# Kernel tuning notes

Measured on AMD Instinct MI355X. Metric: run time of the kernel, lower is better.

Reference implementation:

```python
import jax, jax.numpy as jnp
import numpy as np

N, D, K = 65536, 4096, 16
LN_EPS = 1e-5
SN_EPS = 1e-12
MIN_NORM = 1e-15


def setup_inputs() -> dict:
    key = jax.random.key(0)
    k1, k2, k3, k4 = jax.random.split(key, 4)
    return {
        "x": jax.random.normal(k1, (N, D), dtype=jnp.float32),
        "gamma": jnp.ones((D,), dtype=jnp.float32),
        "beta": jnp.zeros((D,), dtype=jnp.float32),
        "W": jax.random.normal(k2, (K, D), dtype=jnp.float32) * 0.02,
        "u": jax.random.normal(k3, (K,), dtype=jnp.float32),
        "log_scale": jnp.float32(-2.0),
    }


def _l2_normalize(v, eps=SN_EPS):
    return v / (jnp.linalg.norm(v) + eps)


def reference(x, gamma, beta, W, u, log_scale):
    # LayerNorm over last dim
    mean = jnp.mean(x, axis=-1, keepdims=True)
    var = jnp.mean(jnp.square(x - mean), axis=-1, keepdims=True)
    xn = (x - mean) * jax.lax.rsqrt(var + LN_EPS) * gamma + beta

    # spectral norm of W: one power iteration (torch spectral_norm forward)
    v = _l2_normalize(W.T @ u)           # [D]
    u_new = _l2_normalize(W @ v)         # [K]
    sigma = u_new @ (W @ v)              # scalar, top singular value estimate
    W_sn = W / sigma

    # linear (no bias) + learned scale
    vout = xn @ W_sn.T                   # [N, K]
    scale = jax.nn.sigmoid(log_scale) * 0.5
    vout = vout * scale

    # Poincare ball expmap0 with c=1: tanh(||v||) * v / ||v||
    vnorm = jnp.maximum(jnp.linalg.norm(vout, axis=-1, keepdims=True), MIN_NORM)
    return jnp.tanh(vnorm) * vout / vnorm
```

## Files before the change

### kernel.cpp

```cpp
#include <hip/hip_runtime.h>
#include <hip/hip_bf16.h>


#define ND 4096
#define NK 16
#define NROWS 65536

using f32x4  = __attribute__((ext_vector_type(4))) float;
using bf16x8 = __attribute__((ext_vector_type(8))) short;

#define GWB_OFF  0u
#define T_OFF    131072u
#define PART_OFF 147456u
#define SC_OFF   149568u

__device__ __forceinline__ unsigned short f2bf(float f) {
    union { __hip_bfloat16 h; unsigned short u; } cv;
    cv.h = __float2bfloat16(f);
    return cv.u;
}

__global__ __launch_bounds__(256) void prep_a(
    const float* __restrict__ W, const float* __restrict__ gamma,
    const float* __restrict__ beta, const float* __restrict__ u,
    float* __restrict__ ws_t, unsigned short* __restrict__ ws_gwb,
    float* __restrict__ ws_part)
{
    const int d = blockIdx.x * 256 + threadIdx.x;
    float uu[NK];
#pragma unroll
    for (int k = 0; k < NK; ++k) uu[k] = u[k];
    const float g = gamma[d], b = beta[d];
    float w[NK];
#pragma unroll
    for (int k = 0; k < NK; ++k) w[k] = W[k * ND + d];
    float t = 0.f;
#pragma unroll
    for (int k = 0; k < NK; ++k) t = fmaf(w[k], uu[k], t);
    ws_t[d] = t;
    const int c8 = d >> 3, j = d & 7;
#pragma unroll
    for (int k = 0; k < NK; ++k) ws_gwb[(c8 * NK + k) * 8 + j] = f2bf(g * w[k]);

    __shared__ float red[256][34];
    red[threadIdx.x][0] = t * t;
#pragma unroll
    for (int k = 0; k < NK; ++k) {
        red[threadIdx.x][1 + k]  = g * w[k];
        red[threadIdx.x][17 + k] = b * w[k];
    }
    __syncthreads();
    for (int off = 128; off > 0; off >>= 1) {
        if (threadIdx.x < off)
            for (int v = 0; v < 33; ++v)
                red[threadIdx.x][v] += red[threadIdx.x + off][v];
        __syncthreads();
    }
    if (threadIdx.x < 33) ws_part[blockIdx.x * 33 + threadIdx.x] = red[0][threadIdx.x];
}

__global__ __launch_bounds__(256) void prep_b(
    const float* __restrict__ W, const float* __restrict__ ws_t,
    const float* __restrict__ ws_part, const float* __restrict__ log_scale,
    float* __restrict__ sc)
{
    __shared__ float tot[33];
    __shared__ float red[256][17];
    const int tid = threadIdx.x;
    if (tid < 33) {
        float s = 0.f;
        for (int b = 0; b < 16; ++b) s += ws_part[b * 33 + tid];
        tot[tid] = s;
    }
    __syncthreads();
    const float inv_nt = 1.0f / (sqrtf(tot[0]) + 1e-12f);
    float sp[NK];
#pragma unroll
    for (int k = 0; k < NK; ++k) sp[k] = 0.f;
    for (int j = 0; j < 16; ++j) {
        const int d = tid * 16 + j;
        const float vd = ws_t[d] * inv_nt;
#pragma unroll
        for (int k = 0; k < NK; ++k) sp[k] = fmaf(W[k * ND + d], vd, sp[k]);
    }
#pragma unroll
    for (int k = 0; k < NK; ++k) red[tid][k] = sp[k];
    __syncthreads();
    for (int off = 128; off > 0; off >>= 1) {
        if (tid < off)
            for (int v = 0; v < NK; ++v) red[tid][v] += red[tid + off][v];
        __syncthreads();
    }
    if (tid == 0) {
        float ns2 = 0.f;
        for (int k = 0; k < NK; ++k) ns2 += red[0][k] * red[0][k];
        const float sigma = ns2 / (sqrtf(ns2) + 1e-12f);
        const float ls = log_scale[0];
        const float scale = 0.5f / (1.0f + expf(-ls));
        sc[0] = scale / sigma;
        for (int k = 0; k < NK; ++k) { sc[1 + k] = tot[1 + k]; sc[17 + k] = tot[17 + k]; }
    }
}

__global__ __launch_bounds__(1024, 4) void hyp_main(
    const float* __restrict__ x, const unsigned short* __restrict__ gwb_g,
    const float* __restrict__ sc, float* __restrict__ out)
{
    __shared__ unsigned short gwb[ND * NK];
    {
        const uint4* src = (const uint4*)gwb_g;
        uint4* dst = (uint4*)gwb;
#pragma unroll
        for (int i = 0; i < 8; ++i)
            dst[threadIdx.x + i * 1024] = src[threadIdx.x + i * 1024];
    }
    __syncthreads();

    const int lane = threadIdx.x & 63;
    const int wid  = threadIdx.x >> 6;
    const int tile = (blockIdx.x << 4) + wid;
    const int lr = lane & 15;
    const int lc = lane >> 4;

    const float* xp = x + (size_t)(tile * 16 + lr) * ND + lc * 8;
    const unsigned short* lp = gwb + lane * 8;

    f32x4 acc = {0.f, 0.f, 0.f, 0.f};
    float s1 = 0.f, s2 = 0.f;

#pragma unroll 4
    for (int c = 0; c < ND; c += 32) {
        f32x4 xa = *(const f32x4*)(xp + c);
        f32x4 xb = *(const f32x4*)(xp + c + 4);
        bf16x8 a;
        a[0] = (short)f2bf(xa[0]); a[1] = (short)f2bf(xa[1]);
        a[2] = (short)f2bf(xa[2]); a[3] = (short)f2bf(xa[3]);
        a[4] = (short)f2bf(xb[0]); a[5] = (short)f2bf(xb[1]);
        a[6] = (short)f2bf(xb[2]); a[7] = (short)f2bf(xb[3]);
        s1 += ((xa[0] + xa[1]) + (xa[2] + xa[3])) + ((xb[0] + xb[1]) + (xb[2] + xb[3]));
        s2 = fmaf(xa[0], xa[0], s2); s2 = fmaf(xa[1], xa[1], s2);
        s2 = fmaf(xa[2], xa[2], s2); s2 = fmaf(xa[3], xa[3], s2);
        s2 = fmaf(xb[0], xb[0], s2); s2 = fmaf(xb[1], xb[1], s2);
        s2 = fmaf(xb[2], xb[2], s2); s2 = fmaf(xb[3], xb[3], s2);
        bf16x8 b = *(const bf16x8*)(lp + c * 16);
        acc = __builtin_amdgcn_mfma_f32_16x16x32_bf16(a, b, acc, 0, 0, 0);
    }

    s1 += __shfl_xor(s1, 16); s1 += __shfl_xor(s1, 32);
    s2 += __shfl_xor(s2, 16); s2 += __shfl_xor(s2, 32);
    const float mean = s1 * (1.0f / ND);
    const float var  = s2 * (1.0f / ND) - mean * mean;
    const float rstd = rsqrtf(var + 1e-5f);

    const float coef = sc[0];
    const float gk = sc[1 + lr];
    const float bk = sc[17 + lr];

    float vout[4];
#pragma unroll
    for (int j = 0; j < 4; ++j) {
        const int r = lc * 4 + j;
        const float m_r  = __shfl(mean, r);
        const float rs_r = __shfl(rstd, r);
        vout[j] = coef * (fmaf(-m_r, gk, acc[j]) * rs_r + bk);
    }

    float nsq[4];
#pragma unroll
    for (int j = 0; j < 4; ++j) nsq[j] = vout[j] * vout[j];
#pragma unroll
    for (int m = 1; m < 16; m <<= 1) {
#pragma unroll
        for (int j = 0; j < 4; ++j) nsq[j] += __shfl_xor(nsq[j], m);
    }

#pragma unroll
    for (int j = 0; j < 4; ++j) {
        float nv = sqrtf(nsq[j]);
        nv = fmaxf(nv, 1e-15f);
        const float fac = tanhf(nv) / nv;
        out[(size_t)(tile * 16 + lc * 4 + j) * NK + lr] = vout[j] * fac;
    }
}

extern "C" void kernel_launch(void* const* d_in, const int* in_sizes, int n_in,
                              void* d_out, int out_size, void* d_ws, size_t ws_size,
                              hipStream_t stream) {
    const float* x     = (const float*)d_in[0];
    const float* gamma = (const float*)d_in[1];
    const float* beta  = (const float*)d_in[2];
    const float* W     = (const float*)d_in[3];
    const float* u     = (const float*)d_in[4];
    const float* ls    = (const float*)d_in[5];

    char* ws = (char*)d_ws;
    unsigned short* ws_gwb = (unsigned short*)(ws + GWB_OFF);
    float* ws_t    = (float*)(ws + T_OFF);
    float* ws_part = (float*)(ws + PART_OFF);
    float* sc      = (float*)(ws + SC_OFF);
    float* out     = (float*)d_out;

    prep_a<<<16, 256, 0, stream>>>(W, gamma, beta, u, ws_t, ws_gwb, ws_part);
    prep_b<<<1, 256, 0, stream>>>(W, ws_t, ws_part, ls, sc);
    hyp_main<<<256, 1024, 0, stream>>>(x, ws_gwb, sc, out);
}
```

Measured before the change: 208.6 us.

## Merge prep kernels into one block and prefetch x with nontemporal loads

The two prep kernels become a single 1024-thread kernel that uses wave shuffles for its reductions, which removes one launch and a global round trip of intermediates. In the main kernel the first x chunk is loaded before the shared-memory weight copy, and the loop is software-pipelined so the next chunk is loaded ahead of the current MFMA. x loads and output stores use nontemporal hints. A single-block prep gives less parallelism for that stage, and the manual prefetch raises register pressure.

```diff
diff --git a/kernel.cpp b/kernel.cpp
--- a/kernel.cpp
+++ b/kernel.cpp
@@ -10,9 +10,7 @@
 using bf16x8 = __attribute__((ext_vector_type(8))) short;
 
 #define GWB_OFF  0u
-#define T_OFF    131072u
-#define PART_OFF 147456u
-#define SC_OFF   149568u
+#define SC_OFF   131072u
 
 __device__ __forceinline__ unsigned short f2bf(float f) {
     union { __hip_bfloat16 h; unsigned short u; } cv;
@@ -20,84 +18,98 @@
     return cv.u;
 }
 
-__global__ __launch_bounds__(256) void prep_a(
+__global__ __launch_bounds__(1024) void prep(
     const float* __restrict__ W, const float* __restrict__ gamma,
     const float* __restrict__ beta, const float* __restrict__ u,
-    float* __restrict__ ws_t, unsigned short* __restrict__ ws_gwb,
-    float* __restrict__ ws_part)
+    const float* __restrict__ log_scale,
+    unsigned short* __restrict__ ws_gwb, float* __restrict__ sc)
 {
-    const int d = blockIdx.x * 256 + threadIdx.x;
+    const int tid = threadIdx.x;
+    const int lane = tid & 63, wid = tid >> 6;
+    __shared__ float t_sh[ND];
+    __shared__ float wred[16][34];
+    __shared__ float tot[34];
+
     float uu[NK];
 #pragma unroll
     for (int k = 0; k < NK; ++k) uu[k] = u[k];
-    const float g = gamma[d], b = beta[d];
-    float w[NK];
-#pragma unroll
-    for (int k = 0; k < NK; ++k) w[k] = W[k * ND + d];
-    float t = 0.f;
-#pragma unroll
-    for (int k = 0; k < NK; ++k) t = fmaf(w[k], uu[k], t);
-    ws_t[d] = t;
-    const int c8 = d >> 3, j = d & 7;
-#pragma unroll
-    for (int k = 0; k < NK; ++k) ws_gwb[(c8 * NK + k) * 8 + j] = f2bf(g * w[k]);
-
-    __shared__ float red[256][34];
-    red[threadIdx.x][0] = t * t;
+
+    const int d0 = tid * 4;
+    const f32x4 g4 = *(const f32x4*)(gamma + d0);
+    const f32x4 b4 = *(const f32x4*)(beta + d0);
+
+    f32x4 t4 = {0.f, 0.f, 0.f, 0.f};
+    float G[NK], B[NK];
+    const int c8 = tid >> 1;
+    const int j0 = (tid & 1) * 4;
 #pragma unroll
     for (int k = 0; k < NK; ++k) {
-        red[threadIdx.x][1 + k]  = g * w[k];
-        red[threadIdx.x][17 + k] = b * w[k];
-    }
-    __syncthreads();
-    for (int off = 128; off > 0; off >>= 1) {
-        if (threadIdx.x < off)
-            for (int v = 0; v < 33; ++v)
-                red[threadIdx.x][v] += red[threadIdx.x + off][v];
-        __syncthreads();
-    }
-    if (threadIdx.x < 33) ws_part[blockIdx.x * 33 + threadIdx.x] = red[0][threadIdx.x];
-}
-
-__global__ __launch_bounds__(256) void prep_b(
-    const float* __restrict__ W, const float* __restrict__ ws_t,
-    const float* __restrict__ ws_part, const float* __restrict__ log_scale,
-    float* __restrict__ sc)
-{
-    __shared__ float tot[33];
-    __shared__ float red[256][17];
-    const int tid = threadIdx.x;
+        const f32x4 w4 = *(const f32x4*)(W + k * ND + d0);
+        t4[0] = fmaf(w4[0], uu[k], t4[0]);
+        t4[1] = fmaf(w4[1], uu[k], t4[1]);
+        t4[2] = fmaf(w4[2], uu[k], t4[2]);
+        t4[3] = fmaf(w4[3], uu[k], t4[3]);
+        const float gw0 = g4[0]*w4[0], gw1 = g4[1]*w4[1], gw2 = g4[2]*w4[2], gw3 = g4[3]*w4[3];
+        G[k] = (gw0 + gw1) + (gw2 + gw3);
+        B[k] = (b4[0]*w4[0] + b4[1]*w4[1]) + (b4[2]*w4[2] + b4[3]*w4[3]);
+        ushort4 st;
+        st.x = f2bf(gw0); st.y = f2bf(gw1); st.z = f2bf(gw2); st.w = f2bf(gw3);
+        *(ushort4*)(ws_gwb + (c8 * NK + k) * 8 + j0) = st;
+    }
+    *(f32x4*)(t_sh + d0) = t4;
+    float nt2 = (t4[0]*t4[0] + t4[1]*t4[1]) + (t4[2]*t4[2] + t4[3]*t4[3]);
+#pragma unroll
+    for (int m = 1; m < 64; m <<= 1) {
+        nt2 += __shfl_xor(nt2, m);
+#pragma unroll
+        for (int k = 0; k < NK; ++k) {
+            G[k] += __shfl_xor(G[k], m);
+            B[k] += __shfl_xor(B[k], m);
+        }
+    }
+    if (lane == 0) {
+        wred[wid][0] = nt2;
+#pragma unroll
+        for (int k = 0; k < NK; ++k) { wred[wid][1 + k] = G[k]; wred[wid][17 + k] = B[k]; }
+    }
+    __syncthreads();
     if (tid < 33) {
         float s = 0.f;
-        for (int b = 0; b < 16; ++b) s += ws_part[b * 33 + tid];
+        for (int w = 0; w < 16; ++w) s += wred[w][tid];
         tot[tid] = s;
     }
     __syncthreads();
     const float inv_nt = 1.0f / (sqrtf(tot[0]) + 1e-12f);
+    f32x4 tv = *(const f32x4*)(t_sh + d0);
+    tv[0] *= inv_nt; tv[1] *= inv_nt; tv[2] *= inv_nt; tv[3] *= inv_nt;
     float sp[NK];
 #pragma unroll
-    for (int k = 0; k < NK; ++k) sp[k] = 0.f;
-    for (int j = 0; j < 16; ++j) {
-        const int d = tid * 16 + j;
-        const float vd = ws_t[d] * inv_nt;
-#pragma unroll
-        for (int k = 0; k < NK; ++k) sp[k] = fmaf(W[k * ND + d], vd, sp[k]);
-    }
-#pragma unroll
-    for (int k = 0; k < NK; ++k) red[tid][k] = sp[k];
-    __syncthreads();
-    for (int off = 128; off > 0; off >>= 1) {
-        if (tid < off)
-            for (int v = 0; v < NK; ++v) red[tid][v] += red[tid + off][v];
-        __syncthreads();
-    }
+    for (int k = 0; k < NK; ++k) {
+        const f32x4 w4 = *(const f32x4*)(W + k * ND + d0);
+        sp[k] = (w4[0]*tv[0] + w4[1]*tv[1]) + (w4[2]*tv[2] + w4[3]*tv[3]);
+    }
+#pragma unroll
+    for (int m = 1; m < 64; m <<= 1) {
+#pragma unroll
+        for (int k = 0; k < NK; ++k) sp[k] += __shfl_xor(sp[k], m);
+    }
+    __syncthreads();
+    if (lane == 0) {
+#pragma unroll
+        for (int k = 0; k < NK; ++k) wred[wid][k] = sp[k];
+    }
+    __syncthreads();
     if (tid == 0) {
         float ns2 = 0.f;
-        for (int k = 0; k < NK; ++k) ns2 += red[0][k] * red[0][k];
+        for (int k = 0; k < NK; ++k) {
+            float s = 0.f;
+            for (int w = 0; w < 16; ++w) s += wred[w][k];
+            ns2 += s * s;
+        }
         const float sigma = ns2 / (sqrtf(ns2) + 1e-12f);
-        const float ls = log_scale[0];
-        const float scale = 0.5f / (1.0f + expf(-ls));
+        const float scale = 0.5f / (1.0f + expf(-log_scale[0]));
         sc[0] = scale / sigma;
+#pragma unroll
         for (int k = 0; k < NK; ++k) { sc[1 + k] = tot[1 + k]; sc[17 + k] = tot[17 + k]; }
     }
 }
@@ -107,14 +119,6 @@
     const float* __restrict__ sc, float* __restrict__ out)
 {
     __shared__ unsigned short gwb[ND * NK];
-    {
-        const uint4* src = (const uint4*)gwb_g;
-        uint4* dst = (uint4*)gwb;
-#pragma unroll
-        for (int i = 0; i < 8; ++i)
-            dst[threadIdx.x + i * 1024] = src[threadIdx.x + i * 1024];
-    }
-    __syncthreads();
 
     const int lane = threadIdx.x & 63;
     const int wid  = threadIdx.x >> 6;
@@ -125,26 +129,50 @@
     const float* xp = x + (size_t)(tile * 16 + lr) * ND + lc * 8;
     const unsigned short* lp = gwb + lane * 8;
 
+    f32x4 xa = __builtin_nontemporal_load((const f32x4*)xp);
+    f32x4 xb = __builtin_nontemporal_load((const f32x4*)(xp + 4));
+
+    {
+        const uint4* src = (const uint4*)gwb_g;
+        uint4* dst = (uint4*)gwb;
+#pragma unroll
+        for (int i = 0; i < 8; ++i)
+            dst[threadIdx.x + i * 1024] = src[threadIdx.x + i * 1024];
+    }
+    __syncthreads();
+
+    const float coef = sc[0];
+    const float gk = sc[1 + lr];
+    const float bk = sc[17 + lr];
+
     f32x4 acc = {0.f, 0.f, 0.f, 0.f};
     float s1 = 0.f, s2 = 0.f;
 
+#define PROCESS(XA, XB, CC) do {                                          \
+        bf16x8 afrag;                                                     \
+        afrag[0] = (short)f2bf(XA[0]); afrag[1] = (short)f2bf(XA[1]);     \
+        afrag[2] = (short)f2bf(XA[2]); afrag[3] = (short)f2bf(XA[3]);     \
+        afrag[4] = (short)f2bf(XB[0]); afrag[5] = (short)f2bf(XB[1]);     \
+        afrag[6] = (short)f2bf(XB[2]); afrag[7] = (short)f2bf(XB[3]);     \
+        s1 += ((XA[0] + XA[1]) + (XA[2] + XA[3]))                         \
+            + ((XB[0] + XB[1]) + (XB[2] + XB[3]));                        \
+        s2 = fmaf(XA[0], XA[0], s2); s2 = fmaf(XA[1], XA[1], s2);         \
+        s2 = fmaf(XA[2], XA[2], s2); s2 = fmaf(XA[3], XA[3], s2);         \
+        s2 = fmaf(XB[0], XB[0], s2); s2 = fmaf(XB[1], XB[1], s2);         \
+        s2 = fmaf(XB[2], XB[2], s2); s2 = fmaf(XB[3], XB[3], s2);         \
+        bf16x8 bfrag = *(const bf16x8*)(lp + (CC) * 16);                  \
+        acc = __builtin_amdgcn_mfma_f32_16x16x32_bf16(afrag, bfrag, acc, 0, 0, 0); \
+    } while (0)
+
 #pragma unroll 4
-    for (int c = 0; c < ND; c += 32) {
-        f32x4 xa = *(const f32x4*)(xp + c);
-        f32x4 xb = *(const f32x4*)(xp + c + 4);
-        bf16x8 a;
-        a[0] = (short)f2bf(xa[0]); a[1] = (short)f2bf(xa[1]);
-        a[2] = (short)f2bf(xa[2]); a[3] = (short)f2bf(xa[3]);
-        a[4] = (short)f2bf(xb[0]); a[5] = (short)f2bf(xb[1]);
-        a[6] = (short)f2bf(xb[2]); a[7] = (short)f2bf(xb[3]);
-        s1 += ((xa[0] + xa[1]) + (xa[2] + xa[3])) + ((xb[0] + xb[1]) + (xb[2] + xb[3]));
-        s2 = fmaf(xa[0], xa[0], s2); s2 = fmaf(xa[1], xa[1], s2);
-        s2 = fmaf(xa[2], xa[2], s2); s2 = fmaf(xa[3], xa[3], s2);
-        s2 = fmaf(xb[0], xb[0], s2); s2 = fmaf(xb[1], xb[1], s2);
-        s2 = fmaf(xb[2], xb[2], s2); s2 = fmaf(xb[3], xb[3], s2);
-        bf16x8 b = *(const bf16x8*)(lp + c * 16);
-        acc = __builtin_amdgcn_mfma_f32_16x16x32_bf16(a, b, acc, 0, 0, 0);
-    }
+    for (int c = 0; c < ND - 32; c += 32) {
+        f32x4 na = __builtin_nontemporal_load((const f32x4*)(xp + c + 32));
+        f32x4 nb = __builtin_nontemporal_load((const f32x4*)(xp + c + 36));
+        PROCESS(xa, xb, c);
+        xa = na; xb = nb;
+    }
+    PROCESS(xa, xb, ND - 32);
+#undef PROCESS
 
     s1 += __shfl_xor(s1, 16); s1 += __shfl_xor(s1, 32);
     s2 += __shfl_xor(s2, 16); s2 += __shfl_xor(s2, 32);
@@ -152,10 +180,6 @@
     const float var  = s2 * (1.0f / ND) - mean * mean;
     const float rstd = rsqrtf(var + 1e-5f);
 
-    const float coef = sc[0];
-    const float gk = sc[1 + lr];
-    const float bk = sc[17 + lr];
-
     float vout[4];
 #pragma unroll
     for (int j = 0; j < 4; ++j) {
@@ -179,7 +203,8 @@
         float nv = sqrtf(nsq[j]);
         nv = fmaxf(nv, 1e-15f);
         const float fac = tanhf(nv) / nv;
-        out[(size_t)(tile * 16 + lc * 4 + j) * NK + lr] = vout[j] * fac;
+        __builtin_nontemporal_store(vout[j] * fac,
+            out + (size_t)(tile * 16 + lc * 4 + j) * NK + lr);
     }
 }
 
@@ -195,12 +220,9 @@
 
     char* ws = (char*)d_ws;
     unsigned short* ws_gwb = (unsigned short*)(ws + GWB_OFF);
-    float* ws_t    = (float*)(ws + T_OFF);
-    float* ws_part = (float*)(ws + PART_OFF);
     float* sc      = (float*)(ws + SC_OFF);
     float* out     = (float*)d_out;
 
-    prep_a<<<16, 256, 0, stream>>>(W, gamma, beta, u, ws_t, ws_gwb, ws_part);
-    prep_b<<<1, 256, 0, stream>>>(W, ws_t, ws_part, ls, sc);
+    prep<<<1, 1024, 0, stream>>>(W, gamma, beta, u, ls, ws_gwb, sc);
     hyp_main<<<256, 1024, 0, stream>>>(x, ws_gwb, sc, out);
 }
```

Result: slower. 213.5 us (+2.4%).
